# Optimization experiments

Measured on AMD Instinct MI355X. Metric: run time of the kernel, lower is better.

## Reference

```python
import jax, jax.numpy as jnp
import numpy as np

B, L, C = 256, 256, 128
HID, H = 128, 4
D = HID // H            # 32
NUM_LAYERS = 2
NEG_SLOPE = 0.2
LN_EPS = 1e-5


def setup_inputs() -> dict:
    key = jax.random.key(0)
    ks = jax.random.split(key, 16)
    E = 4096
    x = jax.random.normal(ks[0], (B, L, C), dtype=jnp.float32)
    edge_index = jax.random.randint(ks[1], (2, E), 0, C, dtype=jnp.int64)
    s_in = 1.0 / np.sqrt(L)
    s_h = 1.0 / np.sqrt(HID)
    return {
        "x": x,
        "edge_index": edge_index,
        "emb_W": jax.random.normal(ks[2], (L, HID), jnp.float32) * s_in,
        "emb_b": jnp.zeros((HID,), jnp.float32),
        "lin_l_W": jax.random.normal(ks[3], (NUM_LAYERS, HID, HID), jnp.float32) * s_h,
        "lin_l_b": jnp.zeros((NUM_LAYERS, HID), jnp.float32),
        "lin_r_W": jax.random.normal(ks[4], (NUM_LAYERS, HID, HID), jnp.float32) * s_h,
        "lin_r_b": jnp.zeros((NUM_LAYERS, HID), jnp.float32),
        "att": jax.random.normal(ks[5], (NUM_LAYERS, H, D), jnp.float32) * (1.0 / np.sqrt(D)),
        "gat_bias": jnp.zeros((NUM_LAYERS, HID), jnp.float32),
        "ln_gamma": jnp.ones((NUM_LAYERS, HID), jnp.float32),
        "ln_beta": jnp.zeros((NUM_LAYERS, HID), jnp.float32),
        "proj_W": jax.random.normal(ks[6], (HID, L), jnp.float32) * s_h,
        "proj_b": jnp.zeros((L,), jnp.float32),
    }


def _batch_edges(edge_index):
    # replicate single-graph edges per batch sample with node offsets, then add self loops
    E = edge_index.shape[1]
    off = jnp.repeat(jnp.arange(B, dtype=edge_index.dtype) * C, E)
    src = jnp.tile(edge_index[0], B) + off
    dst = jnp.tile(edge_index[1], B) + off
    loop = jnp.arange(B * C, dtype=edge_index.dtype)
    return jnp.concatenate([src, loop]), jnp.concatenate([dst, loop])


def _layer_norm(x, g, b):
    mu = jnp.mean(x, axis=-1, keepdims=True)
    var = jnp.mean(jnp.square(x - mu), axis=-1, keepdims=True)
    return (x - mu) * jax.lax.rsqrt(var + LN_EPS) * g + b


def _gatv2(x, src, dst, Wl, bl, Wr, br, a, bias):
    N = x.shape[0]
    xl = (x @ Wl + bl).reshape(N, H, D)   # source-side transform
    xr = (x @ Wr + br).reshape(N, H, D)   # target-side transform
    e = jax.nn.leaky_relu(xl[src] + xr[dst], NEG_SLOPE)   # (E', H, D)
    logits = jnp.einsum('ehd,hd->eh', e, a)               # (E', H)
    m = jax.ops.segment_max(logits, dst, num_segments=N)
    p = jnp.exp(logits - m[dst])
    s = jax.ops.segment_sum(p, dst, num_segments=N)
    alpha = p / (s[dst] + 1e-16)
    out = jax.ops.segment_sum(xl[src] * alpha[:, :, None], dst, num_segments=N)
    return out.reshape(N, HID) + bias, alpha


def reference(x, edge_index, emb_W, emb_b, lin_l_W, lin_l_b, lin_r_W, lin_r_b,
              att, gat_bias, ln_gamma, ln_beta, proj_W, proj_b):
    src, dst = _batch_edges(edge_index)
    # (B, L, C) -> nodes are channels: (B*C, L) -> embed to HID
    h = x.transpose(0, 2, 1).reshape(B * C, L) @ emb_W + emb_b
    alpha = None
    for i in range(NUM_LAYERS):
        new_h, alpha = _gatv2(h, src, dst, lin_l_W[i], lin_l_b[i],
                              lin_r_W[i], lin_r_b[i], att[i], gat_bias[i])
        new_h = jax.nn.elu(new_h)
        h = h + new_h
        h = _layer_norm(h, ln_gamma[i], ln_beta[i])
        # dropout: eval mode, identity
    # attention map (to_dense_adj semantics: adj[b, src%C, dst%C] = mean_h(alpha), then transpose)
    b_idx = src // C
    dense = jnp.zeros((B, C, C), x.dtype).at[b_idx, src % C, dst % C].add(alpha.mean(axis=-1))
    attn_map = dense.transpose(0, 2, 1)
    out = (h @ proj_W + proj_b).reshape(B, C, L).transpose(0, 2, 1)  # (B, L, C)
    return out, attn_map
```

## Files before the change

### kernel.cpp

```cpp
#include <hip/hip_runtime.h>
#include <hip/hip_fp16.h>
#include <math.h>

#define BB 256
#define LL 256
#define CC 128
#define HIDD 128
#define HH 4
#define DD 32
#define EE 4096
#define NN (BB*CC)
#define LN_EPS 1e-5f

typedef short bf16x8 __attribute__((ext_vector_type(8)));
typedef _Float16 f16x8 __attribute__((ext_vector_type(8)));
typedef float f32x4 __attribute__((ext_vector_type(4)));

__device__ __forceinline__ float red64(float p) {
    p += __shfl_xor(p, 32);
    p += __shfl_xor(p, 16);
    p += __shfl_xor(p, 8);
    p += __shfl_xor(p, 4);
    p += __shfl_xor(p, 2);
    p += __shfl_xor(p, 1);
    return p;
}
__device__ __forceinline__ unsigned bfr(float f) {
    unsigned x = __float_as_uint(f);
    return (x + 0x7FFFu + ((x >> 16) & 1u)) >> 16;
}
__device__ __forceinline__ unsigned pack2(float a, float b) { return bfr(a) | (bfr(b) << 16); }
__device__ __forceinline__ float b2f(unsigned u) { return __uint_as_float(u << 16); }
__device__ __forceinline__ __half2 u2h(unsigned u) { __half2 r; *(unsigned*)&r = u; return r; }
__device__ __forceinline__ unsigned h2u(__half2 h) { return *(unsigned*)&h; }

__device__ __forceinline__ void stage_bf16_rm(ushort* lds, const ushort* src, int ldm, int t) {
    #pragma unroll
    for (int i = 0; i < 8; ++i) {
        int flat = i*256 + t;
        int r = flat >> 4, c = flat & 15;
        uint4 pk = *(const uint4*)(src + (size_t)r*ldm + c*8);
        *(uint4*)&lds[((r*16) + (c ^ (r & 7)))*8] = pk;
    }
}
__device__ __forceinline__ void mfma_tile_128(const ushort* Als, const ushort* Bls,
                                              f32x4 acc[2][8], int w, int lane) {
    int mr = lane & 15, quad = lane >> 4;
    #pragma unroll
    for (int ks = 0; ks < 4; ++ks) {
        int ca = ks*4 + quad;
        bf16x8 a[2], b[8];
        #pragma unroll
        for (int mf = 0; mf < 2; ++mf) {
            int m = w*32 + mf*16 + mr;
            a[mf] = *(const bf16x8*)&Als[((m*16) + (ca ^ (m & 7)))*8];
        }
        #pragma unroll
        for (int nf = 0; nf < 8; ++nf) {
            int n = nf*16 + mr;
            b[nf] = *(const bf16x8*)&Bls[((n*16) + (ca ^ (n & 7)))*8];
        }
        #pragma unroll
        for (int mf = 0; mf < 2; ++mf)
            #pragma unroll
            for (int nf = 0; nf < 8; ++nf)
                acc[mf][nf] = __builtin_amdgcn_mfma_f32_16x16x32_bf16(a[mf], b[nf], acc[mf][nf], 0, 0, 0);
    }
}
#define ZERO_ACC(acc) { _Pragma("unroll") for (int i_=0;i_<2;++i_) { _Pragma("unroll") for (int j_=0;j_<8;++j_) acc[i_][j_] = (f32x4){0.f,0.f,0.f,0.f}; } }

__global__ __launch_bounds__(256) void prep_weights(const float* __restrict__ emb_W,
                                                    const float* __restrict__ lWl,
                                                    const float* __restrict__ lWr,
                                                    const float* __restrict__ pW,
                                                    ushort* __restrict__ WembT,
                                                    ushort* __restrict__ WlrT,
                                                    ushort* __restrict__ WpT) {
    int gid = blockIdx.x * 256 + threadIdx.x;
    float v[8];
    if (gid < 4096) {
        int f = gid >> 5, ch = gid & 31;
        #pragma unroll
        for (int j = 0; j < 8; ++j) v[j] = emb_W[(size_t)(ch*8 + j)*HIDD + f];
        uint4 pk; pk.x = pack2(v[0],v[1]); pk.y = pack2(v[2],v[3]);
        pk.z = pack2(v[4],v[5]); pk.w = pack2(v[6],v[7]);
        *(uint4*)&WembT[(size_t)f*LL + ch*8] = pk;
    } else if (gid < 12288) {
        int g = gid - 4096;
        int mat = g >> 11, f = (g >> 4) & 127, ch = g & 15;
        const float* src = ((mat & 1) ? lWr : lWl) + (size_t)(mat >> 1)*HIDD*HIDD;
        #pragma unroll
        for (int j = 0; j < 8; ++j) v[j] = src[(size_t)(ch*8 + j)*HIDD + f];
        uint4 pk; pk.x = pack2(v[0],v[1]); pk.y = pack2(v[2],v[3]);
        pk.z = pack2(v[4],v[5]); pk.w = pack2(v[6],v[7]);
        *(uint4*)&WlrT[(size_t)mat*HIDD*HIDD + (size_t)f*HIDD + ch*8] = pk;
    } else {
        int g = gid - 12288;
        int l = g >> 4, ch = g & 15;
        #pragma unroll
        for (int j = 0; j < 8; ++j) v[j] = pW[(size_t)(ch*8 + j)*LL + l];
        uint4 pk; pk.x = pack2(v[0],v[1]); pk.y = pack2(v[2],v[3]);
        pk.z = pack2(v[4],v[5]); pk.w = pack2(v[6],v[7]);
        *(uint4*)&WpT[(size_t)l*HIDD + ch*8] = pk;
    }
}

__global__ __launch_bounds__(256) void build_lnm(const int* __restrict__ edge,
                                                 __half* __restrict__ lnmT) {
    __shared__ int cnt[CC*CC];
    int t = threadIdx.x;
    for (int i = t; i < CC*CC; i += 256) cnt[i] = 0;
    __syncthreads();
    for (int j = t; j < EE; j += 256) {
        int s = edge[j], d = edge[EE + j];
        atomicAdd(&cnt[s*CC + d], 1);
    }
    __syncthreads();
    for (int i = t; i < CC*CC; i += 256) {
        int c = cnt[i] + (((i >> 7) == (i & 127)) ? 1 : 0);
        lnmT[i] = __float2half(c > 0 ? logf((float)c) : -30000.f);
    }
}

__global__ __launch_bounds__(256) void embed_mfma(const float* __restrict__ x,
                                                  const ushort* __restrict__ WembT,
                                                  const float* __restrict__ bias,
                                                  ushort* __restrict__ hout) {
    __shared__ __align__(16) ushort Als[128*16*8];
    __shared__ __align__(16) ushort Bls[128*16*8];
    int b = blockIdx.x;
    int t = threadIdx.x, lane = t & 63, w = t >> 6;
    const float* xb = x + (size_t)b * LL * CC;
    f32x4 acc[2][8];
    ZERO_ACC(acc)
    #pragma unroll
    for (int kh = 0; kh < 2; ++kh) {
        if (kh) __syncthreads();
        #pragma unroll
        for (int i = 0; i < 8; ++i) {
            int flat = i*256 + t;
            int r = flat >> 4, cc = flat & 15;
            float v[8];
            #pragma unroll
            for (int j = 0; j < 8; ++j)
                v[j] = xb[(size_t)(kh*128 + cc*8 + j)*CC + r];
            uint4 pk; pk.x = pack2(v[0],v[1]); pk.y = pack2(v[2],v[3]);
            pk.z = pack2(v[4],v[5]); pk.w = pack2(v[6],v[7]);
            *(uint4*)&Als[((r*16) + (cc ^ (r & 7)))*8] = pk;
        }
        stage_bf16_rm(Bls, WembT + kh*128, LL, t);
        __syncthreads();
        mfma_tile_128(Als, Bls, acc, w, lane);
    }
    int mr = lane & 15, quad = lane >> 4;
    #pragma unroll
    for (int nf = 0; nf < 8; ++nf) {
        int f = nf*16 + mr;
        float bv = bias[f];
        #pragma unroll
        for (int mf = 0; mf < 2; ++mf)
            #pragma unroll
            for (int r = 0; r < 4; ++r) {
                int node = w*32 + mf*16 + quad*4 + r;
                hout[((size_t)b*CC + node)*HIDD + f] = (ushort)bfr(acc[mf][nf][r] + bv);
            }
    }
}

__global__ __launch_bounds__(256) void lin_mfma(const ushort* __restrict__ hmat,
                                                const ushort* __restrict__ WlT,
                                                const ushort* __restrict__ WrT,
                                                const float* __restrict__ bl,
                                                const float* __restrict__ br,
                                                __half* __restrict__ xlT,
                                                __half* __restrict__ xrT) {
    __shared__ __align__(16) ushort Als[128*16*8];
    __shared__ __align__(16) ushort Bls[128*16*8];
    int b = blockIdx.x;
    int t = threadIdx.x, lane = t & 63, w = t >> 6;
    int mr = lane & 15, quad = lane >> 4;
    stage_bf16_rm(Als, hmat + (size_t)b*CC*HIDD, HIDD, t);
    #pragma unroll
    for (int lr = 0; lr < 2; ++lr) {
        if (lr) __syncthreads();
        stage_bf16_rm(Bls, lr ? WrT : WlT, HIDD, t);
        __syncthreads();
        f32x4 acc[2][8];
        ZERO_ACC(acc)
        mfma_tile_128(Als, Bls, acc, w, lane);
        const float* bias = lr ? br : bl;
        __half* out = lr ? xrT : xlT;
        #pragma unroll
        for (int nf = 0; nf < 8; ++nf) {
            int f = nf*16 + mr;
            float bv = bias[f];
            int h = f >> 5, d = f & 31;
            #pragma unroll
            for (int mf = 0; mf < 2; ++mf)
                #pragma unroll
                for (int r = 0; r < 4; ++r) {
                    int node = w*32 + mf*16 + quad*4 + r;
                    out[(((size_t)b*HH + h)*CC + node)*DD + d] = __float2half(acc[mf][nf][r] + bv);
                }
        }
    }
}

__global__ __launch_bounds__(256) void gat_dense(const __half* __restrict__ xl_h,
                                                 const __half* __restrict__ xr_h,
                                                 const __half* __restrict__ lnmT,
                                                 const float* __restrict__ att,
                                                 __half* __restrict__ xagg,
                                                 __half* __restrict__ Pws) {
    __shared__ __align__(16) __half xl_lds[CC*DD];
    __shared__ __align__(16) __half xlT_swz[DD*16*8];
    __shared__ __align__(16) __half P[CC*16*8];
    __shared__ float Slq[CC];
    __shared__ float rpart[2][CC];
    __shared__ float spart[2][CC];
    __shared__ float isv[CC];

    int bh = blockIdx.x;
    int h = bh & 3;
    int t = threadIdx.x;
    int sg = t >> 7, dst = t & 127;
    int lane = t & 63, w = t >> 6;

    {
        const uint4* sp = (const uint4*)(xl_h + (size_t)bh * CC * DD);
        uint4* dp = (uint4*)xl_lds;
        dp[t] = sp[t];
        dp[t + 256] = sp[t + 256];
    }
    __half2 qa2[16], xr2[16];
    const float* ag = att + h*DD;
    #pragma unroll
    for (int c = 0; c < 8; ++c) {
        float4 av = *(const float4*)&ag[c*4];
        qa2[2*c+0] = __floats2half2_rn(0.4f*av.x, 0.4f*av.y);
        qa2[2*c+1] = __floats2half2_rn(0.4f*av.z, 0.4f*av.w);
    }
    float Srq = 0.f;
    {
        uint4 X[4];
        const uint4* xp = (const uint4*)(xr_h + ((size_t)bh*CC + dst)*DD);
        #pragma unroll
        for (int c = 0; c < 4; ++c) X[c] = xp[c];
        const __half2* xv = (const __half2*)X;
        #pragma unroll
        for (int i = 0; i < 16; ++i) {
            xr2[i] = xv[i];
            __half2 p = __hmul2(qa2[i], xr2[i]);
            Srq += __low2float(p) + __high2float(p);
        }
    }
    __syncthreads();

    if (t < CC) {
        uint4 R[4];
        const uint4* rp = (const uint4*)&xl_lds[t*DD];
        #pragma unroll
        for (int c = 0; c < 4; ++c) R[c] = rp[c];
        const __half2* rv = (const __half2*)R;
        __half2 s = __floats2half2_rn(0.f, 0.f);
        #pragma unroll
        for (int i = 0; i < 16; ++i) s = __hfma2(qa2[i], rv[i], s);
        Slq[t] = __low2float(s) + __high2float(s);
    }
    for (int i = t; i < 512; i += 256) {
        int f = i >> 4, c = i & 15;
        __align__(16) __half v[8];
        #pragma unroll
        for (int e = 0; e < 8; ++e) v[e] = xl_lds[(c*8 + e)*DD + f];
        *(uint4*)&xlT_swz[((f*16) + (c ^ (f & 7)))*8] = *(uint4*)v;
    }
    __syncthreads();

    const __half* lnm_row = lnmT + dst;
    float pmax = -3.0e38f;
    #pragma unroll 2
    for (int jc = 0; jc < 8; ++jc) {
        int chunk = sg*8 + jc;
        __align__(16) __half lv[8];
        #pragma unroll
        for (int e = 0; e < 8; ++e) {
            int src = chunk*8 + e;
            float lnm = __half2float(lnm_row[(size_t)src*CC]);
            uint4 R[4];
            const uint4* rp = (const uint4*)&xl_lds[src*DD];
            #pragma unroll
            for (int c = 0; c < 4; ++c) R[c] = rp[c];
            const __half2* xv = (const __half2*)R;
            __half2 a0 = __floats2half2_rn(0.f,0.f), a1 = a0, a2 = a0, a3 = a0;
            #pragma unroll
            for (int q = 0; q < 4; ++q) {
                a0 = __hfma2(qa2[4*q+0], __habs2(__hadd2(xv[4*q+0], xr2[4*q+0])), a0);
                a1 = __hfma2(qa2[4*q+1], __habs2(__hadd2(xv[4*q+1], xr2[4*q+1])), a1);
                a2 = __hfma2(qa2[4*q+2], __habs2(__hadd2(xv[4*q+2], xr2[4*q+2])), a2);
                a3 = __hfma2(qa2[4*q+3], __habs2(__hadd2(xv[4*q+3], xr2[4*q+3])), a3);
            }
            __half2 ts = __hadd2(__hadd2(a0, a1), __hadd2(a2, a3));
            float T = __low2float(ts) + __high2float(ts);
            float l = fmaf(1.5f, Slq[src] + Srq, T) + lnm;
            pmax = fmaxf(pmax, l);
            lv[e] = __float2half(l);
        }
        *(uint4*)&P[((dst*16) + (chunk ^ (dst & 7)))*8] = *(uint4*)lv;
    }

    rpart[sg][dst] = pmax;
    __syncthreads();
    float m = fmaxf(rpart[0][dst], rpart[1][dst]);
    float ssum = 0.f;
    #pragma unroll
    for (int jc = 0; jc < 8; ++jc) {
        int chunk = sg*8 + jc;
        uint4* slot = (uint4*)&P[((dst*16) + (chunk ^ (dst & 7)))*8];
        uint4 u = *slot;
        __half2* ph = (__half2*)&u;
        #pragma unroll
        for (int i = 0; i < 4; ++i) {
            float e0 = __expf(__low2float(ph[i]) - m);
            float e1 = __expf(__high2float(ph[i]) - m);
            ssum += e0 + e1;
            ph[i] = __floats2half2_rn(e0, e1);
        }
        *slot = u;
    }
    spart[sg][dst] = ssum;
    __syncthreads();
    if (sg == 0) isv[dst] = 1.f / (spart[0][dst] + spart[1][dst] + 1e-16f);
    __syncthreads();

    int mr = lane & 15, quad = lane >> 4;
    f32x4 acc[2][2];
    #pragma unroll
    for (int i = 0; i < 2; ++i)
        #pragma unroll
        for (int j = 0; j < 2; ++j) acc[i][j] = (f32x4){0.f,0.f,0.f,0.f};
    #pragma unroll
    for (int ks = 0; ks < 4; ++ks) {
        int ca = ks*4 + quad;
        f16x8 a[2], bfrag[2];
        #pragma unroll
        for (int mf = 0; mf < 2; ++mf) {
            int mm = w*32 + mf*16 + mr;
            a[mf] = *(const f16x8*)&P[((mm*16) + (ca ^ (mm & 7)))*8];
        }
        #pragma unroll
        for (int nf = 0; nf < 2; ++nf) {
            int nn = nf*16 + mr;
            bfrag[nf] = *(const f16x8*)&xlT_swz[((nn*16) + (ca ^ (nn & 7)))*8];
        }
        #pragma unroll
        for (int mf = 0; mf < 2; ++mf)
            #pragma unroll
            for (int nf = 0; nf < 2; ++nf)
                acc[mf][nf] = __builtin_amdgcn_mfma_f32_16x16x32_f16(a[mf], bfrag[nf], acc[mf][nf], 0, 0, 0);
    }
    {
        int b = bh >> 2;
        #pragma unroll
        for (int mf = 0; mf < 2; ++mf)
            #pragma unroll
            for (int r = 0; r < 4; ++r) {
                int drow = w*32 + mf*16 + quad*4 + r;
                float is = isv[drow];
                #pragma unroll
                for (int nf = 0; nf < 2; ++nf) {
                    int f = nf*16 + mr;
                    xagg[(((size_t)b*CC + drow)*HH + h)*DD + f] =
                        __float2half(acc[mf][nf][r] * is);
                }
            }
    }

    if (Pws) {
        __half* pg = Pws + (size_t)bh * CC * CC;
        for (int i = t; i < CC*CC/2; i += 256) {
            int dd = i >> 6, sp = i & 63;
            int src = sp*2;
            int chunk = (src >> 3) ^ (dd & 7);
            __half2 v = *(const __half2*)&P[((dd*16) + chunk)*8 + (src & 7)];
            float is = isv[dd];
            *(__half2*)&pg[dd*CC + src] =
                __floats2half2_rn(__low2float(v)*is, __high2float(v)*is);
        }
    }
}

__global__ __launch_bounds__(256) void gat_epilogue(const __half* __restrict__ xagg,
                                                    const float* __restrict__ gbias,
                                                    const float* __restrict__ ln_g,
                                                    const float* __restrict__ ln_b,
                                                    const __half* __restrict__ Pws,
                                                    ushort* __restrict__ hmat,
                                                    float* __restrict__ attn_out) {
    __shared__ float wred[4], wred2[4];
    int t = threadIdx.x;
    int nl = t >> 7, f = t & 127;
    int node = blockIdx.x*2 + nl;
    int b = node >> 7, dstc = node & 127;

    float o = __half2float(xagg[(size_t)node*HIDD + f]) + gbias[f];
    o = o > 0.f ? o : (__expf(o) - 1.f);
    float hv = b2f((unsigned)hmat[(size_t)node*HIDD + f]) + o;

    float sum = red64(hv);
    if ((t & 63) == 0) wred[t >> 6] = sum;
    __syncthreads();
    float mean = (wred[nl*2] + wred[nl*2+1]) * 0.0078125f;
    float d = hv - mean;
    float q = red64(d * d);
    if ((t & 63) == 0) wred2[t >> 6] = q;
    __syncthreads();
    float var = (wred2[nl*2] + wred2[nl*2+1]) * 0.0078125f;
    hmat[(size_t)node*HIDD + f] = (ushort)bfr(d * rsqrtf(var + LN_EPS) * ln_g[f] + ln_b[f]);

    if (attn_out) {
        float a = 0.f;
        #pragma unroll
        for (int hh = 0; hh < HH; ++hh)
            a += __half2float(Pws[(((size_t)(b*HH + hh)*CC) + dstc)*CC + f]);
        attn_out[(size_t)node*CC + f] = 0.25f * a;
    }
}

__global__ __launch_bounds__(256) void proj_mfma(const ushort* __restrict__ hmat,
                                                 const ushort* __restrict__ WpT,
                                                 const float* __restrict__ bias,
                                                 float* __restrict__ out) {
    __shared__ __align__(16) ushort Als[128*16*8];
    __shared__ __align__(16) ushort Bls[128*16*8];
    int l0 = blockIdx.x * 128;
    int b  = blockIdx.y;
    int t = threadIdx.x, lane = t & 63, w = t >> 6;
    f32x4 acc[2][8];
    ZERO_ACC(acc)
    stage_bf16_rm(Als, WpT + (size_t)l0*HIDD, HIDD, t);
    stage_bf16_rm(Bls, hmat + (size_t)b*CC*HIDD, HIDD, t);
    __syncthreads();
    mfma_tile_128(Als, Bls, acc, w, lane);
    int mr = lane & 15, quad = lane >> 4;
    #pragma unroll
    for (int nf = 0; nf < 8; ++nf) {
        int c = nf*16 + mr;
        #pragma unroll
        for (int mf = 0; mf < 2; ++mf)
            #pragma unroll
            for (int r = 0; r < 4; ++r) {
                int l = l0 + w*32 + mf*16 + quad*4 + r;
                out[((size_t)b*LL + l)*CC + c] = acc[mf][nf][r] + bias[l];
            }
    }
}

extern "C" void kernel_launch(void* const* d_in, const int* in_sizes, int n_in,
                              void* d_out, int out_size, void* d_ws, size_t ws_size,
                              hipStream_t stream) {
    const float* x        = (const float*)d_in[0];
    const int*   edge     = (const int*)d_in[1];
    const float* emb_W    = (const float*)d_in[2];
    const float* emb_b    = (const float*)d_in[3];
    const float* lin_l_W  = (const float*)d_in[4];
    const float* lin_l_b  = (const float*)d_in[5];
    const float* lin_r_W  = (const float*)d_in[6];
    const float* lin_r_b  = (const float*)d_in[7];
    const float* att      = (const float*)d_in[8];
    const float* gat_bias = (const float*)d_in[9];
    const float* ln_g     = (const float*)d_in[10];
    const float* ln_b     = (const float*)d_in[11];
    const float* proj_W   = (const float*)d_in[12];
    const float* proj_b   = (const float*)d_in[13];

    ushort* h     = (ushort*)d_ws;
    __half* xl_h  = (__half*)(h + (size_t)NN * HIDD);
    __half* xr_h  = xl_h + (size_t)NN * HIDD;
    __half* xagg  = xr_h + (size_t)NN * HIDD;
    __half* Pws   = xagg + (size_t)NN * HIDD;
    __half* lnmT  = Pws + (size_t)BB * HH * CC * CC;
    ushort* WembT = (ushort*)(lnmT + (size_t)CC * CC);
    ushort* WlrT  = WembT + (size_t)CC*LL;
    ushort* WpT   = WlrT + (size_t)4*HIDD*HIDD;

    float* out0 = (float*)d_out;
    float* attn = out0 + (size_t)BB * LL * CC;

    build_lnm<<<1, 256, 0, stream>>>(edge, lnmT);
    prep_weights<<<64, 256, 0, stream>>>(emb_W, lin_l_W, lin_r_W, proj_W, WembT, WlrT, WpT);
    embed_mfma<<<BB, 256, 0, stream>>>(x, WembT, emb_b, h);
    for (int layer = 0; layer < 2; ++layer) {
        lin_mfma<<<BB, 256, 0, stream>>>(h,
            WlrT + (size_t)(layer*2 + 0)*HIDD*HIDD,
            WlrT + (size_t)(layer*2 + 1)*HIDD*HIDD,
            lin_l_b + layer*HIDD, lin_r_b + layer*HIDD,
            xl_h, xr_h);
        gat_dense<<<BB*HH, 256, 0, stream>>>(xl_h, xr_h, lnmT,
            att + layer*HIDD, xagg, (layer == 1) ? Pws : nullptr);
        gat_epilogue<<<NN/2, 256, 0, stream>>>(xagg,
            gat_bias + layer*HIDD, ln_g + layer*HIDD, ln_b + layer*HIDD,
            (layer == 1) ? Pws : nullptr, h, (layer == 1) ? attn : nullptr);
    }
    proj_mfma<<<dim3(2, BB), 256, 0, stream>>>(h, WpT, proj_b, out0);
}
```

Baseline: 283.5 us.

## Split fused GAT kernel into logits/softmax and PV MFMA kernels via global P

Splits gat_dense into gat_logits, which computes logits and the softmax in registers and writes normalized P to global memory, and gat_pv, which reads P and runs the MFMA aggregation. The edge-count log-mask is stored dst-major so each thread reads it with contiguous 16-byte loads. Removing the large LDS P buffer and adding occupancy bounds aims to raise occupancy. In exchange, P now goes through global memory in both layers instead of only the last, adding a 32 MB write plus read per layer and an extra launch.

```diff
diff --git a/kernel.cpp b/kernel.cpp
--- a/kernel.cpp
+++ b/kernel.cpp
@@ -106,7 +106,7 @@
 }
 
 __global__ __launch_bounds__(256) void build_lnm(const int* __restrict__ edge,
-                                                 __half* __restrict__ lnmT) {
+                                                 __half* __restrict__ lnm_ds) {
     __shared__ int cnt[CC*CC];
     int t = threadIdx.x;
     for (int i = t; i < CC*CC; i += 256) cnt[i] = 0;
@@ -116,9 +116,10 @@
         atomicAdd(&cnt[s*CC + d], 1);
     }
     __syncthreads();
-    for (int i = t; i < CC*CC; i += 256) {
-        int c = cnt[i] + (((i >> 7) == (i & 127)) ? 1 : 0);
-        lnmT[i] = __float2half(c > 0 ? logf((float)c) : -30000.f);
+    for (int o = t; o < CC*CC; o += 256) {
+        int dstc = o >> 7, srcc = o & 127;
+        int c = cnt[srcc*CC + dstc] + ((srcc == dstc) ? 1 : 0);
+        lnm_ds[o] = __float2half(c > 0 ? logf((float)c) : -30000.f);
     }
 }
 
@@ -206,25 +207,20 @@
     }
 }
 
-__global__ __launch_bounds__(256) void gat_dense(const __half* __restrict__ xl_h,
-                                                 const __half* __restrict__ xr_h,
-                                                 const __half* __restrict__ lnmT,
-                                                 const float* __restrict__ att,
-                                                 __half* __restrict__ xagg,
-                                                 __half* __restrict__ Pws) {
+__global__ __launch_bounds__(256, 4) void gat_logits(const __half* __restrict__ xl_h,
+                                                     const __half* __restrict__ xr_h,
+                                                     const __half* __restrict__ lnm_ds,
+                                                     const float* __restrict__ att,
+                                                     __half* __restrict__ Pg) {
     __shared__ __align__(16) __half xl_lds[CC*DD];
-    __shared__ __align__(16) __half xlT_swz[DD*16*8];
-    __shared__ __align__(16) __half P[CC*16*8];
     __shared__ float Slq[CC];
     __shared__ float rpart[2][CC];
     __shared__ float spart[2][CC];
-    __shared__ float isv[CC];
 
     int bh = blockIdx.x;
     int h = bh & 3;
     int t = threadIdx.x;
     int sg = t >> 7, dst = t & 127;
-    int lane = t & 63, w = t >> 6;
 
     {
         const uint4* sp = (const uint4*)(xl_h + (size_t)bh * CC * DD);
@@ -267,25 +263,21 @@
         for (int i = 0; i < 16; ++i) s = __hfma2(qa2[i], rv[i], s);
         Slq[t] = __low2float(s) + __high2float(s);
     }
-    for (int i = t; i < 512; i += 256) {
-        int f = i >> 4, c = i & 15;
-        __align__(16) __half v[8];
-        #pragma unroll
-        for (int e = 0; e < 8; ++e) v[e] = xl_lds[(c*8 + e)*DD + f];
-        *(uint4*)&xlT_swz[((f*16) + (c ^ (f & 7)))*8] = *(uint4*)v;
-    }
-    __syncthreads();
-
-    const __half* lnm_row = lnmT + dst;
+    __syncthreads();
+
+    const __half* lrow = lnm_ds + (size_t)dst*CC + sg*64;
+    float fSrq = 1.5f * Srq;
+    __half2 lv2[32];
     float pmax = -3.0e38f;
-    #pragma unroll 2
+    #pragma unroll
     for (int jc = 0; jc < 8; ++jc) {
         int chunk = sg*8 + jc;
-        __align__(16) __half lv[8];
+        uint4 lu = *(const uint4*)&lrow[jc*8];
+        const __half* lnmv = (const __half*)&lu;
+        float lf[8];
         #pragma unroll
         for (int e = 0; e < 8; ++e) {
             int src = chunk*8 + e;
-            float lnm = __half2float(lnm_row[(size_t)src*CC]);
             uint4 R[4];
             const uint4* rp = (const uint4*)&xl_lds[src*DD];
             #pragma unroll
@@ -301,11 +293,14 @@
             }
             __half2 ts = __hadd2(__hadd2(a0, a1), __hadd2(a2, a3));
             float T = __low2float(ts) + __high2float(ts);
-            float l = fmaf(1.5f, Slq[src] + Srq, T) + lnm;
+            float l = fmaf(1.5f, Slq[src], fSrq + T) + __half2float(lnmv[e]);
             pmax = fmaxf(pmax, l);
-            lv[e] = __float2half(l);
-        }
-        *(uint4*)&P[((dst*16) + (chunk ^ (dst & 7)))*8] = *(uint4*)lv;
+            lf[e] = l;
+        }
+        lv2[jc*4+0] = __floats2half2_rn(lf[0], lf[1]);
+        lv2[jc*4+1] = __floats2half2_rn(lf[2], lf[3]);
+        lv2[jc*4+2] = __floats2half2_rn(lf[4], lf[5]);
+        lv2[jc*4+3] = __floats2half2_rn(lf[6], lf[7]);
     }
 
     rpart[sg][dst] = pmax;
@@ -313,26 +308,63 @@
     float m = fmaxf(rpart[0][dst], rpart[1][dst]);
     float ssum = 0.f;
     #pragma unroll
+    for (int i = 0; i < 32; ++i) {
+        float e0 = __expf(__low2float(lv2[i]) - m);
+        float e1 = __expf(__high2float(lv2[i]) - m);
+        ssum += e0 + e1;
+        lv2[i] = __floats2half2_rn(e0, e1);
+    }
+    spart[sg][dst] = ssum;
+    __syncthreads();
+    float is = 1.f / (spart[0][dst] + spart[1][dst] + 1e-16f);
+
+    __half* pgr = Pg + (size_t)bh*CC*CC + (size_t)dst*CC + sg*64;
+    #pragma unroll
     for (int jc = 0; jc < 8; ++jc) {
-        int chunk = sg*8 + jc;
-        uint4* slot = (uint4*)&P[((dst*16) + (chunk ^ (dst & 7)))*8];
-        uint4 u = *slot;
-        __half2* ph = (__half2*)&u;
+        __align__(16) __half ov[8];
         #pragma unroll
         for (int i = 0; i < 4; ++i) {
-            float e0 = __expf(__low2float(ph[i]) - m);
-            float e1 = __expf(__high2float(ph[i]) - m);
-            ssum += e0 + e1;
-            ph[i] = __floats2half2_rn(e0, e1);
-        }
-        *slot = u;
-    }
-    spart[sg][dst] = ssum;
-    __syncthreads();
-    if (sg == 0) isv[dst] = 1.f / (spart[0][dst] + spart[1][dst] + 1e-16f);
+            __half2 v = lv2[jc*4+i];
+            ov[2*i+0] = __float2half(__low2float(v) * is);
+            ov[2*i+1] = __float2half(__high2float(v) * is);
+        }
+        *(uint4*)&pgr[jc*8] = *(uint4*)ov;
+    }
+}
+
+__global__ __launch_bounds__(256) void gat_pv(const __half* __restrict__ Pg,
+                                              const __half* __restrict__ xl_h,
+                                              __half* __restrict__ xagg) {
+    __shared__ __align__(16) __half xl_lds[CC*DD];
+    __shared__ __align__(16) __half xlT_swz[DD*16*8];
+    int bh = blockIdx.x, h = bh & 3, b = bh >> 2;
+    int t = threadIdx.x, lane = t & 63, w = t >> 6;
+    {
+        const uint4* sp = (const uint4*)(xl_h + (size_t)bh * CC * DD);
+        uint4* dp = (uint4*)xl_lds;
+        dp[t] = sp[t];
+        dp[t + 256] = sp[t + 256];
+    }
+    __syncthreads();
+    for (int i = t; i < 512; i += 256) {
+        int f = i >> 4, c = i & 15;
+        __align__(16) __half v[8];
+        #pragma unroll
+        for (int e = 0; e < 8; ++e) v[e] = xl_lds[(c*8 + e)*DD + f];
+        *(uint4*)&xlT_swz[((f*16) + (c ^ (f & 7)))*8] = *(uint4*)v;
+    }
     __syncthreads();
 
     int mr = lane & 15, quad = lane >> 4;
+    const __half* pb = Pg + (size_t)bh * CC * CC;
+    f16x8 a[2][4];
+    #pragma unroll
+    for (int mf = 0; mf < 2; ++mf) {
+        int dr = w*32 + mf*16 + mr;
+        #pragma unroll
+        for (int ks = 0; ks < 4; ++ks)
+            a[mf][ks] = *(const f16x8*)&pb[(size_t)dr*CC + ks*32 + quad*8];
+    }
     f32x4 acc[2][2];
     #pragma unroll
     for (int i = 0; i < 2; ++i)
@@ -341,12 +373,7 @@
     #pragma unroll
     for (int ks = 0; ks < 4; ++ks) {
         int ca = ks*4 + quad;
-        f16x8 a[2], bfrag[2];
-        #pragma unroll
-        for (int mf = 0; mf < 2; ++mf) {
-            int mm = w*32 + mf*16 + mr;
-            a[mf] = *(const f16x8*)&P[((mm*16) + (ca ^ (mm & 7)))*8];
-        }
+        f16x8 bfrag[2];
         #pragma unroll
         for (int nf = 0; nf < 2; ++nf) {
             int nn = nf*16 + mr;
@@ -356,37 +383,19 @@
         for (int mf = 0; mf < 2; ++mf)
             #pragma unroll
             for (int nf = 0; nf < 2; ++nf)
-                acc[mf][nf] = __builtin_amdgcn_mfma_f32_16x16x32_f16(a[mf], bfrag[nf], acc[mf][nf], 0, 0, 0);
-    }
-    {
-        int b = bh >> 2;
-        #pragma unroll
-        for (int mf = 0; mf < 2; ++mf)
-            #pragma unroll
-            for (int r = 0; r < 4; ++r) {
-                int drow = w*32 + mf*16 + quad*4 + r;
-                float is = isv[drow];
-                #pragma unroll
-                for (int nf = 0; nf < 2; ++nf) {
-                    int f = nf*16 + mr;
-                    xagg[(((size_t)b*CC + drow)*HH + h)*DD + f] =
-                        __float2half(acc[mf][nf][r] * is);
-                }
+                acc[mf][nf] = __builtin_amdgcn_mfma_f32_16x16x32_f16(a[mf][ks], bfrag[nf], acc[mf][nf], 0, 0, 0);
+    }
+    #pragma unroll
+    for (int mf = 0; mf < 2; ++mf)
+        #pragma unroll
+        for (int r = 0; r < 4; ++r) {
+            int drow = w*32 + mf*16 + quad*4 + r;
+            #pragma unroll
+            for (int nf = 0; nf < 2; ++nf) {
+                int f = nf*16 + mr;
+                xagg[(((size_t)b*CC + drow)*HH + h)*DD + f] = __float2half(acc[mf][nf][r]);
             }
-    }
-
-    if (Pws) {
-        __half* pg = Pws + (size_t)bh * CC * CC;
-        for (int i = t; i < CC*CC/2; i += 256) {
-            int dd = i >> 6, sp = i & 63;
-            int src = sp*2;
-            int chunk = (src >> 3) ^ (dd & 7);
-            __half2 v = *(const __half2*)&P[((dd*16) + chunk)*8 + (src & 7)];
-            float is = isv[dd];
-            *(__half2*)&pg[dd*CC + src] =
-                __floats2half2_rn(__low2float(v)*is, __high2float(v)*is);
-        }
-    }
+        }
 }
 
 __global__ __launch_bounds__(256) void gat_epilogue(const __half* __restrict__ xagg,
@@ -477,16 +486,16 @@
     __half* xl_h  = (__half*)(h + (size_t)NN * HIDD);
     __half* xr_h  = xl_h + (size_t)NN * HIDD;
     __half* xagg  = xr_h + (size_t)NN * HIDD;
-    __half* Pws   = xagg + (size_t)NN * HIDD;
-    __half* lnmT  = Pws + (size_t)BB * HH * CC * CC;
-    ushort* WembT = (ushort*)(lnmT + (size_t)CC * CC);
+    __half* Pg    = xagg + (size_t)NN * HIDD;
+    __half* lnm_ds = Pg + (size_t)BB * HH * CC * CC;
+    ushort* WembT = (ushort*)(lnm_ds + (size_t)CC * CC);
     ushort* WlrT  = WembT + (size_t)CC*LL;
     ushort* WpT   = WlrT + (size_t)4*HIDD*HIDD;
 
     float* out0 = (float*)d_out;
     float* attn = out0 + (size_t)BB * LL * CC;
 
-    build_lnm<<<1, 256, 0, stream>>>(edge, lnmT);
+    build_lnm<<<1, 256, 0, stream>>>(edge, lnm_ds);
     prep_weights<<<64, 256, 0, stream>>>(emb_W, lin_l_W, lin_r_W, proj_W, WembT, WlrT, WpT);
     embed_mfma<<<BB, 256, 0, stream>>>(x, WembT, emb_b, h);
     for (int layer = 0; layer < 2; ++layer) {
@@ -495,11 +504,12 @@
             WlrT + (size_t)(layer*2 + 1)*HIDD*HIDD,
             lin_l_b + layer*HIDD, lin_r_b + layer*HIDD,
             xl_h, xr_h);
-        gat_dense<<<BB*HH, 256, 0, stream>>>(xl_h, xr_h, lnmT,
-            att + layer*HIDD, xagg, (layer == 1) ? Pws : nullptr);
+        gat_logits<<<BB*HH, 256, 0, stream>>>(xl_h, xr_h, lnm_ds,
+            att + layer*HIDD, Pg);
+        gat_pv<<<BB*HH, 256, 0, stream>>>(Pg, xl_h, xagg);
         gat_epilogue<<<NN/2, 256, 0, stream>>>(xagg,
             gat_bias + layer*HIDD, ln_g + layer*HIDD, ln_b + layer*HIDD,
-            (layer == 1) ? Pws : nullptr, h, (layer == 1) ? attn : nullptr);
+            (layer == 1) ? Pg : nullptr, h, (layer == 1) ? attn : nullptr);
     }
     proj_mfma<<<dim3(2, BB), 256, 0, stream>>>(h, WpT, proj_b, out0);
 }
```

After: 305.9 us. +7.9%, slower.
